# Kernel optimization log

Hardware: AMD Instinct MI355X
Metric: run time of the kernel (lower is better)

## Reference

```python
import jax, jax.numpy as jnp
import numpy as np

N_HEAD = 12

def setup_inputs() -> dict:
    key = jax.random.key(0)
    k1, k2, k3 = jax.random.split(key, 3)
    B, T, C = 8, 1024, 768
    x = jax.random.normal(k1, (B, T, C), dtype=jnp.float32)
    # Linear weights stored as [in, out] so y = x @ W + b (same math as torch Linear)
    w_attn = jax.random.normal(k2, (C, 3 * C), dtype=jnp.float32) * (1.0 / np.sqrt(C))
    b_attn = jnp.zeros((3 * C,), dtype=jnp.float32)
    w_proj = jax.random.normal(k3, (C, C), dtype=jnp.float32) * (1.0 / np.sqrt(C))
    b_proj = jnp.zeros((C,), dtype=jnp.float32)
    return {"x": x, "w_attn": w_attn, "b_attn": b_attn, "w_proj": w_proj, "b_proj": b_proj}

def reference(x, w_attn, b_attn, w_proj, b_proj):
    B, T, C = x.shape
    H = N_HEAD
    D = C // H
    qkv = x @ w_attn + b_attn                        # [B,T,3C]
    q, k, v = jnp.split(qkv, 3, axis=-1)             # each [B,T,C]
    q = q.reshape(B, T, H, D).transpose(0, 2, 1, 3)  # [B,H,T,D]
    k = k.reshape(B, T, H, D).transpose(0, 2, 1, 3)
    v = v.reshape(B, T, H, D).transpose(0, 2, 1, 3)
    scale = 1.0 / jnp.sqrt(jnp.asarray(D, dtype=x.dtype))
    att = jnp.einsum('bhqd,bhkd->bhqk', q, k) * scale  # [B,H,T,T]
    causal = jnp.tril(jnp.ones((T, T), dtype=bool))    # [T,T]
    att = jnp.where(causal[None, None], att, jnp.asarray(-jnp.inf, dtype=att.dtype))
    att = jax.nn.softmax(att, axis=-1)
    out = jnp.einsum('bhqk,bhkd->bhqd', att, v)        # [B,H,T,D]
    out = out.transpose(0, 2, 1, 3).reshape(B, T, C)
    return out @ w_proj + b_proj
```

## Files before the change

### kernel.cpp

```cpp
#include <hip/hip_runtime.h>
#include <hip/hip_bf16.h>
#include <cmath>

#define B_ 8
#define T_ 1024
#define C_ 768
#define H_ 12
#define D_ 64
#define N3C 2304
#define M_ 8192

typedef __bf16 bf16x4 __attribute__((ext_vector_type(4)));
typedef __bf16 bf16x8 __attribute__((ext_vector_type(8)));
typedef float  f32x4  __attribute__((ext_vector_type(4)));

typedef const __attribute__((address_space(1))) void* gptr_t;
typedef __attribute__((address_space(3))) void* lptr_t;

#define LOG2E 1.44269504088896f

__device__ __forceinline__ bf16x8 cvt_bf16x8(const float4& a, const float4& b) {
    bf16x8 r;
    r[0] = (__bf16)a.x; r[1] = (__bf16)a.y; r[2] = (__bf16)a.z; r[3] = (__bf16)a.w;
    r[4] = (__bf16)b.x; r[5] = (__bf16)b.y; r[6] = (__bf16)b.z; r[7] = (__bf16)b.w;
    return r;
}

__global__ __launch_bounds__(256) void prepass(const float* __restrict__ x,
                                               __bf16* __restrict__ xb,
                                               const float* __restrict__ wa,
                                               __bf16* __restrict__ wat,
                                               const float* __restrict__ wp,
                                               __bf16* __restrict__ wpt) {
    __shared__ float tile[32][33];
    const int bx = blockIdx.x, tid = threadIdx.x;
    if (bx < 3072) {
        int i = (bx * 256 + tid) * 8;
        float4 a = *(const float4*)&x[i];
        float4 b = *(const float4*)&x[i + 4];
        *(bf16x8*)&xb[i] = cvt_bf16x8(a, b);
        return;
    }
    const float* w;
    __bf16* wt;
    int K, N, n0, k0;
    if (bx < 4800) {
        int bb = bx - 3072;
        w = wa; wt = wat; K = 768; N = 2304;
        n0 = (bb % 72) * 32; k0 = (bb / 72) * 32;
    } else {
        int bb = bx - 4800;
        w = wp; wt = wpt; K = 768; N = 768;
        n0 = (bb % 24) * 32; k0 = (bb / 24) * 32;
    }
    int tx = tid & 31, ty = tid >> 5;
#pragma unroll
    for (int i = 0; i < 4; i++)
        tile[ty + i * 8][tx] = w[(size_t)(k0 + ty + i * 8) * N + n0 + tx];
    __syncthreads();
#pragma unroll
    for (int i = 0; i < 4; i++)
        wt[(size_t)(n0 + ty + i * 8) * K + k0 + tx] = (__bf16)tile[tx][ty + i * 8];
}

__global__ __launch_bounds__(256) void qkv_gemm_mfma(const __bf16* __restrict__ A,
                                                     const __bf16* __restrict__ Bt,
                                                     const float* __restrict__ bias,
                                                     __bf16* __restrict__ qb,
                                                     __bf16* __restrict__ kb,
                                                     __bf16* __restrict__ vbt) {
    __shared__ __bf16 smem[2][2][128 * 64];
    const int tid = threadIdx.x;
    const int wave = tid >> 6, lane = tid & 63;
    const int lane15 = lane & 15, quad = lane >> 4;
    const int bid = blockIdx.x;
    const int m0 = ((bid & 7) * 8 + ((bid >> 3) & 7)) * 128;
    const int n0 = (bid >> 6) * 128;
    const int wm = (wave >> 1) * 64, wn = (wave & 1) * 64;
    f32x4 acc[4][4] = {};

#define QSTAGE(KC, BUF)                                                             \
    {                                                                               \
        const int k0s = (KC) * 64;                                                  \
        _Pragma("unroll")                                                           \
        for (int r = 0; r < 4; ++r) {                                               \
            int p = r * 256 + tid;                                                  \
            int mrow = p >> 3, csw = p & 7;                                         \
            int ksrc = (csw ^ (mrow & 7)) * 8;                                      \
            __builtin_amdgcn_global_load_lds(                                       \
                (gptr_t)(A + (size_t)(m0 + mrow) * 768 + k0s + ksrc),               \
                (lptr_t)(&smem[BUF][0][0] + (r * 256 + wave * 64) * 8), 16, 0, 0);  \
            __builtin_amdgcn_global_load_lds(                                       \
                (gptr_t)(Bt + (size_t)(n0 + mrow) * 768 + k0s + ksrc),              \
                (lptr_t)(&smem[BUF][1][0] + (r * 256 + wave * 64) * 8), 16, 0, 0);  \
        }                                                                           \
    }

    QSTAGE(0, 0);
    for (int kc = 0; kc < 12; ++kc) {
        __syncthreads();
        if (kc + 1 < 12) QSTAGE(kc + 1, (kc + 1) & 1);
        const __bf16* As = &smem[kc & 1][0][0];
        const __bf16* Bs = &smem[kc & 1][1][0];
#pragma unroll
        for (int ks = 0; ks < 2; ++ks) {
            bf16x8 af[4], bf[4];
#pragma unroll
            for (int mt = 0; mt < 4; ++mt) {
                int m = wm + mt * 16 + lane15;
                int csw = (ks * 4 + quad) ^ (m & 7);
                af[mt] = *(const bf16x8*)(As + m * 64 + csw * 8);
            }
#pragma unroll
            for (int nt = 0; nt < 4; ++nt) {
                int n = wn + nt * 16 + lane15;
                int csw = (ks * 4 + quad) ^ (n & 7);
                bf[nt] = *(const bf16x8*)(Bs + n * 64 + csw * 8);
            }
#pragma unroll
            for (int mt = 0; mt < 4; ++mt)
#pragma unroll
                for (int nt = 0; nt < 4; ++nt)
                    acc[mt][nt] = __builtin_amdgcn_mfma_f32_16x16x32_bf16(af[mt], bf[nt], acc[mt][nt], 0, 0, 0);
        }
    }
    __syncthreads();

    if (n0 < 1536) {
        const bool isq = (n0 < 768);
        const float sc = isq ? (0.125f * LOG2E) : 1.0f;
#pragma unroll
        for (int nt = 0; nt < 4; ++nt) {
            int n = n0 + wn + nt * 16 + lane15;
            int rem = isq ? n : (n - 768);
            int h = rem >> 6;
            int d = n & 63;
            float bv = bias[n];
            __bf16* dst = isq ? qb : kb;
#pragma unroll
            for (int mt = 0; mt < 4; ++mt) {
#pragma unroll
                for (int reg = 0; reg < 4; ++reg) {
                    int mr = m0 + wm + mt * 16 + quad * 4 + reg;
                    int bb = mr >> 10, t = mr & 1023;
                    dst[(((size_t)bb * H_ + h) * T_ + t) * D_ + d] =
                        (__bf16)((acc[mt][nt][reg] + bv) * sc);
                }
            }
        }
    } else {
        __bf16* vls = &smem[0][0][0];
#pragma unroll
        for (int nt = 0; nt < 4; ++nt) {
            int nl = wn + nt * 16 + lane15;
            float bv = bias[n0 + nl];
#pragma unroll
            for (int mt = 0; mt < 4; ++mt)
#pragma unroll
                for (int reg = 0; reg < 4; ++reg)
                    vls[nl * 136 + wm + mt * 16 + quad * 4 + reg] =
                        (__bf16)(acc[mt][nt][reg] + bv);
        }
        __syncthreads();
        int nl = tid >> 1;
        int t0 = (tid & 1) * 64;
        int n = n0 + nl;
        int h = (n - 1536) >> 6;
        int d = n & 63;
        int bb = m0 >> 10, tg = (m0 & 1023) + t0;
        __bf16* dst = vbt + (((size_t)bb * H_ + h) * D_ + d) * T_ + tg;
        const __bf16* srcl = vls + nl * 136 + t0;
#pragma unroll
        for (int c = 0; c < 8; ++c) {
            bf16x8 v;
#pragma unroll
            for (int i = 0; i < 8; ++i) {
                int s = c * 8 + i;
                v[i] = srcl[(s & 3) * 16 + (s >> 2)];
            }
            *(bf16x8*)(dst + c * 8) = v;
        }
    }
}

__global__ __launch_bounds__(256) void proj_gemm_mfma(const __bf16* __restrict__ A,
                                                      const __bf16* __restrict__ Bt,
                                                      const float* __restrict__ bias,
                                                      float* __restrict__ out) {
    __shared__ __bf16 As[2][128 * 64];
    __shared__ __bf16 Bs[2][64 * 64];
    const int tid = threadIdx.x;
    const int wave = tid >> 6, lane = tid & 63;
    const int lane15 = lane & 15, quad = lane >> 4;
    const int bid = blockIdx.x;
    const int m0 = ((bid & 7) * 8 + ((bid >> 3) & 7)) * 128;
    const int n0 = (bid >> 6) * 64;
    const int wm = wave * 32;
    f32x4 acc[2][4] = {};

#define PSTAGE(KC, BUF)                                                             \
    {                                                                               \
        const int k0s = (KC) * 64;                                                  \
        _Pragma("unroll")                                                           \
        for (int r = 0; r < 4; ++r) {                                               \
            int p = r * 256 + tid;                                                  \
            int mrow = p >> 3, csw = p & 7;                                         \
            int ksrc = (csw ^ (mrow & 7)) * 8;                                      \
            __builtin_amdgcn_global_load_lds(                                       \
                (gptr_t)(A + (size_t)(m0 + mrow) * 768 + k0s + ksrc),               \
                (lptr_t)(&As[BUF][0] + (r * 256 + wave * 64) * 8), 16, 0, 0);       \
        }                                                                           \
        _Pragma("unroll")                                                           \
        for (int r = 0; r < 2; ++r) {                                               \
            int p = r * 256 + tid;                                                  \
            int nrow = p >> 3, csw = p & 7;                                         \
            int ksrc = (csw ^ (nrow & 7)) * 8;                                      \
            __builtin_amdgcn_global_load_lds(                                       \
                (gptr_t)(Bt + (size_t)(n0 + nrow) * 768 + k0s + ksrc),              \
                (lptr_t)(&Bs[BUF][0] + (r * 256 + wave * 64) * 8), 16, 0, 0);       \
        }                                                                           \
    }

    PSTAGE(0, 0);
    for (int kc = 0; kc < 12; ++kc) {
        __syncthreads();
        if (kc + 1 < 12) PSTAGE(kc + 1, (kc + 1) & 1);
        const __bf16* Ac = &As[kc & 1][0];
        const __bf16* Bc = &Bs[kc & 1][0];
#pragma unroll
        for (int ks = 0; ks < 2; ++ks) {
            bf16x8 af[2], bf[4];
#pragma unroll
            for (int mt = 0; mt < 2; ++mt) {
                int m = wm + mt * 16 + lane15;
                int csw = (ks * 4 + quad) ^ (m & 7);
                af[mt] = *(const bf16x8*)(Ac + m * 64 + csw * 8);
            }
#pragma unroll
            for (int nt = 0; nt < 4; ++nt) {
                int n = nt * 16 + lane15;
                int csw = (ks * 4 + quad) ^ (n & 7);
                bf[nt] = *(const bf16x8*)(Bc + n * 64 + csw * 8);
            }
#pragma unroll
            for (int mt = 0; mt < 2; ++mt)
#pragma unroll
                for (int nt = 0; nt < 4; ++nt)
                    acc[mt][nt] = __builtin_amdgcn_mfma_f32_16x16x32_bf16(af[mt], bf[nt], acc[mt][nt], 0, 0, 0);
        }
    }

#pragma unroll
    for (int nt = 0; nt < 4; ++nt) {
        int n = n0 + nt * 16 + lane15;
        float bv = bias[n];
#pragma unroll
        for (int mt = 0; mt < 2; ++mt) {
#pragma unroll
            for (int reg = 0; reg < 4; ++reg) {
                int mr = m0 + wm + mt * 16 + quad * 4 + reg;
                out[(size_t)mr * C_ + n] = acc[mt][nt][reg] + bv;
            }
        }
    }
}

__global__ __launch_bounds__(256) void attn_mfma(const __bf16* __restrict__ qb,
                                                 const __bf16* __restrict__ kb,
                                                 const __bf16* __restrict__ vbt,
                                                 __bf16* __restrict__ ao) {
    __shared__ __bf16 Ks[2][64 * 64];
    __shared__ __bf16 Vts[2][64 * 64];
    __shared__ __bf16 Ps[4 * 32 * 72];

    const int tid = threadIdx.x;
    const int wave = tid >> 6, lane = tid & 63;
    const int lane15 = lane & 15, quad = lane >> 4;
    const int bh = blockIdx.x;
    const int qt = 7 - blockIdx.y;
    const int b = bh / H_, h = bh % H_;
    const int q0 = qt * 128;

    const __bf16* Kb = kb + (size_t)bh * T_ * D_;
    const __bf16* Vb = vbt + (size_t)bh * D_ * T_;
    __bf16* Pw = Ps + wave * 32 * 72;

    bf16x8 qf[2][2];
#pragma unroll
    for (int g = 0; g < 2; ++g) {
        const __bf16* qrow = qb + ((size_t)bh * T_ + q0 + wave * 32 + g * 16 + lane15) * D_ + quad * 8;
        qf[g][0] = *(const bf16x8*)qrow;
        qf[g][1] = *(const bf16x8*)(qrow + 32);
    }

    f32x4 o[2][4] = {};
    float lsum[2][4] = {};

    const int kunits = 2 * qt + 2;

#define ASTAGE(KU, BUF)                                                            \
    {                                                                              \
        const int k0s = (KU) * 64;                                                 \
        _Pragma("unroll")                                                          \
        for (int r = 0; r < 2; ++r) {                                              \
            int p = r * 256 + tid;                                                 \
            int row = p >> 3, c = p & 7;                                           \
            int cs = (c ^ (row & 7)) * 8;                                          \
            __builtin_amdgcn_global_load_lds(                                      \
                (gptr_t)(Kb + (size_t)(k0s + row) * D_ + cs),                      \
                (lptr_t)(&Ks[BUF][0] + (r * 256 + wave * 64) * 8), 16, 0, 0);      \
            __builtin_amdgcn_global_load_lds(                                      \
                (gptr_t)(Vb + (size_t)row * T_ + k0s + cs),                        \
                (lptr_t)(&Vts[BUF][0] + (r * 256 + wave * 64) * 8), 16, 0, 0);     \
        }                                                                          \
    }

    ASTAGE(0, 0);

    for (int ku = 0; ku < kunits; ++ku) {
        __syncthreads();
        if (ku + 1 < kunits) ASTAGE(ku + 1, (ku + 1) & 1);
        const __bf16* Kc = &Ks[ku & 1][0];
        const __bf16* Vc = &Vts[ku & 1][0];
        const int k0 = ku * 64;

        f32x4 s[2][4];
#pragma unroll
        for (int kt = 0; kt < 4; ++kt) {
            int row = kt * 16 + lane15;
            bf16x8 kf0 = *(const bf16x8*)(Kc + row * 64 + ((quad) ^ (row & 7)) * 8);
            bf16x8 kf1 = *(const bf16x8*)(Kc + row * 64 + ((4 + quad) ^ (row & 7)) * 8);
#pragma unroll
            for (int g = 0; g < 2; ++g) {
                f32x4 t = {};
                t = __builtin_amdgcn_mfma_f32_16x16x32_bf16(qf[g][0], kf0, t, 0, 0, 0);
                t = __builtin_amdgcn_mfma_f32_16x16x32_bf16(qf[g][1], kf1, t, 0, 0, 0);
                s[g][kt] = t;
            }
        }

        const bool diag = (ku >= 2 * qt);
#pragma unroll
        for (int g = 0; g < 2; ++g) {
#pragma unroll
            for (int r = 0; r < 4; ++r) {
                bf16x4 pk;
#pragma unroll
                for (int kt = 0; kt < 4; ++kt) {
                    int col = k0 + kt * 16 + lane15;
                    float p = __builtin_amdgcn_exp2f(s[g][kt][r]);
                    if (diag) {
                        int qrow = q0 + wave * 32 + g * 16 + quad * 4 + r;
                        if (col > qrow) p = 0.f;
                    }
                    lsum[g][r] += p;
                    pk[kt] = (__bf16)p;
                }
                *(bf16x4*)(Pw + (g * 16 + quad * 4 + r) * 72 + lane15 * 4) = pk;
            }
        }

        bf16x8 vf[4][2];
#pragma unroll
        for (int dt = 0; dt < 4; ++dt) {
            int row = dt * 16 + lane15;
#pragma unroll
            for (int half = 0; half < 2; ++half)
                vf[dt][half] = *(const bf16x8*)(Vc + row * 64 + ((half * 4 + quad) ^ (row & 7)) * 8);
        }
#pragma unroll
        for (int g = 0; g < 2; ++g) {
#pragma unroll
            for (int half = 0; half < 2; ++half) {
                bf16x8 pf = *(const bf16x8*)(Pw + (g * 16 + lane15) * 72 + half * 32 + quad * 8);
#pragma unroll
                for (int dt = 0; dt < 4; ++dt)
                    o[g][dt] = __builtin_amdgcn_mfma_f32_16x16x32_bf16(pf, vf[dt][half], o[g][dt], 0, 0, 0);
            }
        }
    }

#pragma unroll
    for (int g = 0; g < 2; ++g) {
        float inv[4];
#pragma unroll
        for (int r = 0; r < 4; ++r) {
            float ls = lsum[g][r];
            ls += __shfl_xor(ls, 1);
            ls += __shfl_xor(ls, 2);
            ls += __shfl_xor(ls, 4);
            ls += __shfl_xor(ls, 8);
            inv[r] = 1.0f / ls;
        }
#pragma unroll
        for (int dt = 0; dt < 4; ++dt) {
#pragma unroll
            for (int r = 0; r < 4; ++r) {
                int t = q0 + wave * 32 + g * 16 + quad * 4 + r;
                ao[((size_t)(b * T_ + t)) * C_ + h * 64 + dt * 16 + lane15] =
                    (__bf16)(o[g][dt][r] * inv[r]);
            }
        }
    }
}

extern "C" void kernel_launch(void* const* d_in, const int* in_sizes, int n_in,
                              void* d_out, int out_size, void* d_ws, size_t ws_size,
                              hipStream_t stream) {
    const float* x = (const float*)d_in[0];
    const float* w_attn = (const float*)d_in[1];
    const float* b_attn = (const float*)d_in[2];
    const float* w_proj = (const float*)d_in[3];
    const float* b_proj = (const float*)d_in[4];
    float* out = (float*)d_out;

    __bf16* xb = (__bf16*)d_ws;
    __bf16* wat = xb + (size_t)M_ * C_;
    __bf16* wpt = wat + (size_t)N3C * C_;
    __bf16* qb = wpt + (size_t)C_ * C_;
    __bf16* kb = qb + (size_t)96 * T_ * D_;
    __bf16* vbt = kb + (size_t)96 * T_ * D_;
    __bf16* ao = vbt + (size_t)96 * T_ * D_;

    prepass<<<5376, 256, 0, stream>>>(x, xb, w_attn, wat, w_proj, wpt);
    qkv_gemm_mfma<<<1152, 256, 0, stream>>>(xb, wat, b_attn, qb, kb, vbt);
    attn_mfma<<<dim3(96, 8), 256, 0, stream>>>(qb, kb, vbt, ao);
    proj_gemm_mfma<<<768, 256, 0, stream>>>(ao, wpt, b_proj, out);
}
```

Before: 175.9 us.

## Enlarge QKV GEMM tile to 256x128 and drop LDS double buffering

```diff
diff --git a/kernel.cpp b/kernel.cpp
--- a/kernel.cpp
+++ b/kernel.cpp
@@ -69,44 +69,45 @@
                                                      __bf16* __restrict__ qb,
                                                      __bf16* __restrict__ kb,
                                                      __bf16* __restrict__ vbt) {
-    __shared__ __bf16 smem[2][2][128 * 64];
+    __shared__ __bf16 smem[256 * 64 + 128 * 64];
+    __bf16* As = smem;
+    __bf16* Bs = smem + 256 * 64;
     const int tid = threadIdx.x;
     const int wave = tid >> 6, lane = tid & 63;
     const int lane15 = lane & 15, quad = lane >> 4;
     const int bid = blockIdx.x;
-    const int m0 = ((bid & 7) * 8 + ((bid >> 3) & 7)) * 128;
-    const int n0 = (bid >> 6) * 128;
-    const int wm = (wave >> 1) * 64, wn = (wave & 1) * 64;
-    f32x4 acc[4][4] = {};
-
-#define QSTAGE(KC, BUF)                                                             \
-    {                                                                               \
-        const int k0s = (KC) * 64;                                                  \
-        _Pragma("unroll")                                                           \
-        for (int r = 0; r < 4; ++r) {                                               \
-            int p = r * 256 + tid;                                                  \
-            int mrow = p >> 3, csw = p & 7;                                         \
-            int ksrc = (csw ^ (mrow & 7)) * 8;                                      \
-            __builtin_amdgcn_global_load_lds(                                       \
-                (gptr_t)(A + (size_t)(m0 + mrow) * 768 + k0s + ksrc),               \
-                (lptr_t)(&smem[BUF][0][0] + (r * 256 + wave * 64) * 8), 16, 0, 0);  \
-            __builtin_amdgcn_global_load_lds(                                       \
-                (gptr_t)(Bt + (size_t)(n0 + mrow) * 768 + k0s + ksrc),              \
-                (lptr_t)(&smem[BUF][1][0] + (r * 256 + wave * 64) * 8), 16, 0, 0);  \
-        }                                                                           \
-    }
-
-    QSTAGE(0, 0);
+    const int mi = (bid & 7) * 4 + ((bid >> 3) & 3);
+    const int ni = bid >> 5;
+    const int m0 = mi * 256, n0 = ni * 128;
+    const int wm = (wave >> 1) * 128, wn = (wave & 1) * 64;
+    f32x4 acc[8][4] = {};
+
     for (int kc = 0; kc < 12; ++kc) {
+        const int k0 = kc * 64;
+#pragma unroll
+        for (int r = 0; r < 8; ++r) {
+            int p = r * 256 + tid;
+            int row = p >> 3, c = p & 7;
+            int ks = (c ^ (row & 7)) * 8;
+            __builtin_amdgcn_global_load_lds(
+                (gptr_t)(A + (size_t)(m0 + row) * 768 + k0 + ks),
+                (lptr_t)(As + (r * 256 + wave * 64) * 8), 16, 0, 0);
+        }
+#pragma unroll
+        for (int r = 0; r < 4; ++r) {
+            int p = r * 256 + tid;
+            int row = p >> 3, c = p & 7;
+            int ks = (c ^ (row & 7)) * 8;
+            __builtin_amdgcn_global_load_lds(
+                (gptr_t)(Bt + (size_t)(n0 + row) * 768 + k0 + ks),
+                (lptr_t)(Bs + (r * 256 + wave * 64) * 8), 16, 0, 0);
+        }
         __syncthreads();
-        if (kc + 1 < 12) QSTAGE(kc + 1, (kc + 1) & 1);
-        const __bf16* As = &smem[kc & 1][0][0];
-        const __bf16* Bs = &smem[kc & 1][1][0];
 #pragma unroll
         for (int ks = 0; ks < 2; ++ks) {
-            bf16x8 af[4], bf[4];
-#pragma unroll
-            for (int mt = 0; mt < 4; ++mt) {
+            bf16x8 af[8], bf[4];
+#pragma unroll
+            for (int mt = 0; mt < 8; ++mt) {
                 int m = wm + mt * 16 + lane15;
                 int csw = (ks * 4 + quad) ^ (m & 7);
                 af[mt] = *(const bf16x8*)(As + m * 64 + csw * 8);
@@ -118,16 +119,16 @@
                 bf[nt] = *(const bf16x8*)(Bs + n * 64 + csw * 8);
             }
 #pragma unroll
-            for (int mt = 0; mt < 4; ++mt)
+            for (int mt = 0; mt < 8; ++mt)
 #pragma unroll
                 for (int nt = 0; nt < 4; ++nt)
                     acc[mt][nt] = __builtin_amdgcn_mfma_f32_16x16x32_bf16(af[mt], bf[nt], acc[mt][nt], 0, 0, 0);
         }
-    }
-    __syncthreads();
-
-    if (n0 < 1536) {
-        const bool isq = (n0 < 768);
+        __syncthreads();
+    }
+
+    if (ni < 12) {
+        const bool isq = (ni < 6);
         const float sc = isq ? (0.125f * LOG2E) : 1.0f;
 #pragma unroll
         for (int nt = 0; nt < 4; ++nt) {
@@ -138,7 +139,7 @@
             float bv = bias[n];
             __bf16* dst = isq ? qb : kb;
 #pragma unroll
-            for (int mt = 0; mt < 4; ++mt) {
+            for (int mt = 0; mt < 8; ++mt) {
 #pragma unroll
                 for (int reg = 0; reg < 4; ++reg) {
                     int mr = m0 + wm + mt * 16 + quad * 4 + reg;
@@ -149,36 +150,42 @@
             }
         }
     } else {
-        __bf16* vls = &smem[0][0][0];
-#pragma unroll
-        for (int nt = 0; nt < 4; ++nt) {
-            int nl = wn + nt * 16 + lane15;
-            float bv = bias[n0 + nl];
-#pragma unroll
-            for (int mt = 0; mt < 4; ++mt)
-#pragma unroll
-                for (int reg = 0; reg < 4; ++reg)
-                    vls[nl * 136 + wm + mt * 16 + quad * 4 + reg] =
-                        (__bf16)(acc[mt][nt][reg] + bv);
-        }
-        __syncthreads();
-        int nl = tid >> 1;
-        int t0 = (tid & 1) * 64;
-        int n = n0 + nl;
-        int h = (n - 1536) >> 6;
-        int d = n & 63;
-        int bb = m0 >> 10, tg = (m0 & 1023) + t0;
-        __bf16* dst = vbt + (((size_t)bb * H_ + h) * D_ + d) * T_ + tg;
-        const __bf16* srcl = vls + nl * 136 + t0;
-#pragma unroll
-        for (int c = 0; c < 8; ++c) {
-            bf16x8 v;
-#pragma unroll
-            for (int i = 0; i < 8; ++i) {
-                int s = c * 8 + i;
-                v[i] = srcl[(s & 3) * 16 + (s >> 2)];
-            }
-            *(bf16x8*)(dst + c * 8) = v;
+        __bf16* vls = smem;
+        const int bb = m0 >> 10;
+        const int tg0 = m0 & 1023;
+#pragma unroll
+        for (int ph = 0; ph < 2; ++ph) {
+            if ((wave & 1) == ph) {
+#pragma unroll
+                for (int nt = 0; nt < 4; ++nt) {
+                    int nl = nt * 16 + lane15;
+                    float bv = bias[n0 + ph * 64 + nl];
+#pragma unroll
+                    for (int mt = 0; mt < 8; ++mt)
+#pragma unroll
+                        for (int reg = 0; reg < 4; ++reg)
+                            vls[nl * 264 + wm + mt * 16 + quad * 4 + reg] =
+                                (__bf16)(acc[mt][nt][reg] + bv);
+                }
+            }
+            __syncthreads();
+            int nl = tid >> 2;
+            int t0 = (tid & 3) * 64;
+            int h = (ni - 12) * 2 + ph;
+            int d = nl;
+            __bf16* dst = vbt + (((size_t)bb * H_ + h) * D_ + d) * T_ + tg0 + t0;
+            const __bf16* srcl = vls + nl * 264 + t0;
+#pragma unroll
+            for (int c = 0; c < 8; ++c) {
+                bf16x8 v;
+#pragma unroll
+                for (int i = 0; i < 8; ++i) {
+                    int s = c * 8 + i;
+                    v[i] = srcl[(s & 3) * 16 + (s >> 2)];
+                }
+                *(bf16x8*)(dst + c * 8) = v;
+            }
+            __syncthreads();
         }
     }
 }
@@ -423,7 +430,7 @@
     __bf16* ao = vbt + (size_t)96 * T_ * D_;
 
     prepass<<<5376, 256, 0, stream>>>(x, xb, w_attn, wat, w_proj, wpt);
-    qkv_gemm_mfma<<<1152, 256, 0, stream>>>(xb, wat, b_attn, qb, kb, vbt);
+    qkv_gemm_mfma<<<576, 256, 0, stream>>>(xb, wat, b_attn, qb, kb, vbt);
     attn_mfma<<<dim3(96, 8), 256, 0, stream>>>(qb, kb, vbt, ao);
     proj_gemm_mfma<<<768, 256, 0, stream>>>(ao, wpt, b_proj, out);
 }
```

Result: slower. 206.1 us (+17.2%).
